# Performance work log

Measured on AMD Instinct MI355X. Metric: run time of the kernel, lower is better.

The kernel has to match this reference:

```python
import jax, jax.numpy as jnp
import numpy as np

N, D_IN, R, D_OUT, U = 500000, 128, 256, 64, 10000
EPS = 1e-8


def _vb_layer(m, v, W_mu, W_lv, relu_out):
    # Variational Bayes linear layer, moment propagation:
    #   out_mean = m @ W_mu
    #   out_var  = v @ (W_mu^2 + W_var) + m^2 @ W_var,  W_var = exp(W_lv)
    W_var = jnp.exp(W_lv)
    M = m @ W_mu
    V = v @ (W_mu * W_mu + W_var) + (m * m) @ W_var
    if relu_out:
        gate = (M > 0).astype(M.dtype)
        M = M * gate
        V = V * gate
    return M, V


def setup_inputs() -> dict:
    key = jax.random.key(0)
    ks = jax.random.split(key, 6)
    X = jax.random.normal(ks[0], (N, D_IN), jnp.float32)
    X_idx = jnp.sort(jax.random.randint(ks[1], (N,), 0, U, dtype=jnp.int32))
    W_mu0 = jax.random.normal(ks[2], (D_IN, R), jnp.float32) / np.sqrt(D_IN)
    W_lv0 = jax.random.normal(ks[3], (D_IN, R), jnp.float32) * 0.1 - 4.0
    W_mu1 = jax.random.normal(ks[4], (R, D_OUT), jnp.float32) / np.sqrt(R)
    W_lv1 = jax.random.normal(ks[5], (R, D_OUT), jnp.float32) * 0.1 - 4.0
    return {"X": X, "X_idx": X_idx, "W_mu0": W_mu0, "W_lv0": W_lv0,
            "W_mu1": W_mu1, "W_lv1": W_lv1}


def reference(X, X_idx, W_mu0, W_lv0, W_mu1, W_lv1):
    m, v = _vb_layer(X, jnp.zeros_like(X), W_mu0, W_lv0, True)   # [N, R]
    m, v = _vb_layer(m, v, W_mu1, W_lv1, False)                  # [N, D_OUT]
    v = jnp.maximum(v, EPS)
    inv_v = 1.0 / v
    # precision-weighted aggregation per group id (replaces per-uid loop)
    var_inv_sum = jax.ops.segment_sum(inv_v, X_idx, num_segments=U) + EPS
    mean_sum = jax.ops.segment_sum(m * inv_v, X_idx, num_segments=U)
    emb_var = 1.0 / var_inv_sum          # [U, D_OUT]
    emb_mean = mean_sum * emb_var        # [U, D_OUT]
    return emb_mean, emb_var
```

## Files before the change

### kernel.cpp

```cpp
#include <hip/hip_runtime.h>
#include <stdint.h>

#define N_ROWS 500000
#define U_DIM 10000
#define EPSV 1e-8f
#define NTILES 15625

typedef __attribute__((ext_vector_type(8))) short bf16x8;
typedef __attribute__((ext_vector_type(4))) float f32x4;

__device__ __forceinline__ short f2bf(float f) {
  unsigned u = __float_as_uint(f);
  u += 0x7fffu + ((u >> 16) & 1u);
  return (short)(u >> 16);
}
__device__ __forceinline__ float bf2f(short s) {
  return __uint_as_float(((unsigned)(unsigned short)s) << 16);
}

__global__ void prep_weights(const float* __restrict__ Wmu0,
                             const float* __restrict__ Wlv0,
                             const float* __restrict__ Wmu1,
                             const float* __restrict__ Wlv1,
                             short* __restrict__ wgt) {
  int i = blockIdx.x * blockDim.x + threadIdx.x;
  if (i < 32768) {
    int c = i & 255, k = i >> 8;
    int rc = c >> 5, ct = (c >> 4) & 1, n = c & 15;
    int kt = k >> 5, q = (k >> 3) & 3, u = k & 7;
    int lane = q * 16 + n;
    float mu = Wmu0[k * 256 + c];
    float ev = __expf(Wlv0[k * 256 + c]);
    wgt[((((rc * 2 + 0) * 2 + ct) * 4 + kt) * 64 + lane) * 8 + u] = f2bf(mu);
    wgt[((((rc * 2 + 1) * 2 + ct) * 4 + kt) * 64 + lane) * 8 + u] = f2bf(ev);
  } else if (i < 49152) {
    int i2 = i - 32768;
    int o = i2 & 63, j = i2 >> 6;
    int rc = j >> 5, q = (j >> 3) & 3, u = j & 7;
    int ct1 = o >> 4, n = o & 15;
    int lane = q * 16 + n;
    float mu = Wmu1[j * 64 + o];
    float ev = __expf(Wlv1[j * 64 + o]);
    int b = 65536 + (((rc * 4 + ct1) * 3 + 0) * 64 + lane) * 8 + u;
    wgt[b]        = f2bf(mu);
    wgt[b + 512]  = f2bf(mu * mu + ev);
    wgt[b + 1024] = f2bf(ev);
  }
}

__global__ __launch_bounds__(256, 2) void vb_fused(
    const float* __restrict__ X, const int* __restrict__ Xidx,
    const short* __restrict__ wgt, float* __restrict__ out) {
  __shared__ __align__(16) short stage[2][8192];
  __shared__ short ldsM[4][2][16 * 40];
  __shared__ short ldsV[4][2][16 * 40];

  const int tid  = threadIdx.x;
  const int w    = tid >> 6;
  const int lane = tid & 63;
  const int n    = lane & 15;
  const int q    = lane >> 4;
  const int T    = blockIdx.x * 4 + w;
  const bool active = (T < NTILES);
  const int row0 = active ? T * 32 : (N_ROWS - 32);

  const f32x4 zf4 = {0.f, 0.f, 0.f, 0.f};

  bf16x8 a_m[2][4], a_sq[2][4];
#pragma unroll
  for (int t = 0; t < 2; ++t) {
    const float* xr = X + (size_t)(row0 + t * 16 + n) * 128;
#pragma unroll
    for (int kt = 0; kt < 4; ++kt) {
      float xf[8];
      *(float4*)&xf[0] = *(const float4*)&xr[kt * 32 + q * 8];
      *(float4*)&xf[4] = *(const float4*)&xr[kt * 32 + q * 8 + 4];
#pragma unroll
      for (int u = 0; u < 8; ++u) {
        a_m[t][kt][u]  = f2bf(xf[u]);
        a_sq[t][kt][u] = f2bf(xf[u] * xf[u]);
      }
    }
  }

  f32x4 accm1[2][4], accv1[2][4];
#pragma unroll
  for (int t = 0; t < 2; ++t)
#pragma unroll
    for (int c = 0; c < 4; ++c) { accm1[t][c] = zf4; accv1[t][c] = zf4; }

  const uint4* g4 = (const uint4*)wgt;
  uint4 u0 = g4[tid], u1 = g4[tid + 256], u2 = g4[tid + 512], u3 = g4[tid + 768];

  const int lane8 = lane * 8;

#pragma unroll
  for (int rc = 0; rc < 8; ++rc) {
    uint4* s4 = (uint4*)&stage[rc & 1][0];
    s4[tid] = u0; s4[tid + 256] = u1; s4[tid + 512] = u2; s4[tid + 768] = u3;
    __syncthreads();
    if (rc < 7) {
      const uint4* gn = g4 + (rc + 1) * 1024;
      u0 = gn[tid]; u1 = gn[tid + 256]; u2 = gn[tid + 512]; u3 = gn[tid + 768];
    }

    const short* st = &stage[rc & 1][0];

    f32x4 accm0[2][2], accv0[2][2];
#pragma unroll
    for (int t = 0; t < 2; ++t)
#pragma unroll
      for (int c = 0; c < 2; ++c) { accm0[t][c] = zf4; accv0[t][c] = zf4; }

#pragma unroll
    for (int kt = 0; kt < 4; ++kt) {
#pragma unroll
      for (int ct = 0; ct < 2; ++ct) {
        bf16x8 bm = *(const bf16x8*)&st[((0 * 2 + ct) * 4 + kt) * 512 + lane8];
        bf16x8 bv = *(const bf16x8*)&st[((1 * 2 + ct) * 4 + kt) * 512 + lane8];
#pragma unroll
        for (int t = 0; t < 2; ++t) {
          accm0[t][ct] = __builtin_amdgcn_mfma_f32_16x16x32_bf16(a_m[t][kt],  bm, accm0[t][ct], 0, 0, 0);
          accv0[t][ct] = __builtin_amdgcn_mfma_f32_16x16x32_bf16(a_sq[t][kt], bv, accv0[t][ct], 0, 0, 0);
        }
      }
    }

#pragma unroll
    for (int t = 0; t < 2; ++t) {
#pragma unroll
      for (int ct = 0; ct < 2; ++ct) {
        const int c = ct * 16 + n;
#pragma unroll
        for (int reg = 0; reg < 4; ++reg) {
          float m = accm0[t][ct][reg], v = accv0[t][ct][reg];
          if (!(m > 0.f)) { m = 0.f; v = 0.f; }
          const int row = q * 4 + reg;
          ldsM[w][t][row * 40 + c] = f2bf(m);
          ldsV[w][t][row * 40 + c] = f2bf(v);
        }
      }
    }
    bf16x8 am[2], av[2], asq[2];
#pragma unroll
    for (int t = 0; t < 2; ++t) {
      am[t] = *(const bf16x8*)&ldsM[w][t][n * 40 + q * 8];
      av[t] = *(const bf16x8*)&ldsV[w][t][n * 40 + q * 8];
#pragma unroll
      for (int u = 0; u < 8; ++u) {
        float f = bf2f(am[t][u]);
        asq[t][u] = f2bf(f * f);
      }
    }

    const short* l1b = wgt + 65536 + rc * 6144 + lane8;
#pragma unroll
    for (int ct1 = 0; ct1 < 4; ++ct1) {
      const short* fb = l1b + ct1 * 1536;
      bf16x8 b1 = *(const bf16x8*)&fb[0];
      bf16x8 b2 = *(const bf16x8*)&fb[512];
      bf16x8 b3 = *(const bf16x8*)&fb[1024];
#pragma unroll
      for (int t = 0; t < 2; ++t) {
        accm1[t][ct1] = __builtin_amdgcn_mfma_f32_16x16x32_bf16(am[t],  b1, accm1[t][ct1], 0, 0, 0);
        accv1[t][ct1] = __builtin_amdgcn_mfma_f32_16x16x32_bf16(av[t],  b2, accv1[t][ct1], 0, 0, 0);
        accv1[t][ct1] = __builtin_amdgcn_mfma_f32_16x16x32_bf16(asq[t], b3, accv1[t][ct1], 0, 0, 0);
      }
    }
  }

  if (!active) return;
  float* meanp = out;
  float* varp  = out + U_DIM * 64;
#pragma unroll
  for (int t = 0; t < 2; ++t) {
    int4 idx4 = *(const int4*)&Xidx[row0 + t * 16 + q * 4];
    int uid[4] = {idx4.x, idx4.y, idx4.z, idx4.w};
#pragma unroll
    for (int ct = 0; ct < 4; ++ct) {
      const int o = ct * 16 + n;
      float sm = 0.f, sv = 0.f;
      int cur = uid[0];
#pragma unroll
      for (int reg = 0; reg < 4; ++reg) {
        float v1 = fmaxf(accv1[t][ct][reg], EPSV);
        float inv = 1.0f / v1;
        float mi  = accm1[t][ct][reg] * inv;
        if (uid[reg] != cur) {
          atomicAdd(&meanp[cur * 64 + o], sm);
          atomicAdd(&varp[cur * 64 + o], sv);
          sm = 0.f; sv = 0.f; cur = uid[reg];
        }
        sm += mi; sv += inv;
      }
      atomicAdd(&meanp[cur * 64 + o], sm);
      atomicAdd(&varp[cur * 64 + o], sv);
    }
  }
}

__global__ void finalize(float* __restrict__ out) {
  int i = blockIdx.x * blockDim.x + threadIdx.x;
  if (i < U_DIM * 64) {
    float s = out[U_DIM * 64 + i];
    float var = 1.0f / (s + EPSV);
    out[U_DIM * 64 + i] = var;
    out[i] = out[i] * var;
  }
}

extern "C" void kernel_launch(void* const* d_in, const int* in_sizes, int n_in,
                              void* d_out, int out_size, void* d_ws, size_t ws_size,
                              hipStream_t stream) {
  (void)in_sizes; (void)n_in; (void)out_size; (void)ws_size;
  const float* X    = (const float*)d_in[0];
  const int*   Xidx = (const int*)d_in[1];
  const float* Wmu0 = (const float*)d_in[2];
  const float* Wlv0 = (const float*)d_in[3];
  const float* Wmu1 = (const float*)d_in[4];
  const float* Wlv1 = (const float*)d_in[5];
  float* out = (float*)d_out;
  short* wgt = (short*)d_ws;

  hipMemsetAsync(d_out, 0, (size_t)U_DIM * 64 * 2 * sizeof(float), stream);
  prep_weights<<<192, 256, 0, stream>>>(Wmu0, Wlv0, Wmu1, Wlv1, wgt);
  vb_fused<<<3907, 256, 0, stream>>>(X, Xidx, wgt, out);
  finalize<<<(U_DIM * 64 + 255) / 256, 256, 0, stream>>>(out);
}
```

Measured before the change: 583.7 us.

## Halve per-wave row tile and stream layer-0 weights with global_load_lds

Each wave now processes 16 rows instead of 32, halving accumulator and A-fragment registers, and the grid doubles with launch bounds raised to 3 blocks per CU to increase occupancy. Layer-0 weight staging now uses direct global-to-LDS async loads instead of a register round trip. The trade-off is that every block re-streams the full weight set from L2 for half as many rows, doubling weight traffic and the per-row barrier overhead.

```diff
diff --git a/kernel.cpp b/kernel.cpp
--- a/kernel.cpp
+++ b/kernel.cpp
@@ -4,7 +4,7 @@
 #define N_ROWS 500000
 #define U_DIM 10000
 #define EPSV 1e-8f
-#define NTILES 15625
+#define NT16 31250
 
 typedef __attribute__((ext_vector_type(8))) short bf16x8;
 typedef __attribute__((ext_vector_type(4))) float f32x4;
@@ -48,12 +48,12 @@
   }
 }
 
-__global__ __launch_bounds__(256, 2) void vb_fused(
+__global__ __launch_bounds__(256, 3) void vb_fused(
     const float* __restrict__ X, const int* __restrict__ Xidx,
     const short* __restrict__ wgt, float* __restrict__ out) {
   __shared__ __align__(16) short stage[2][8192];
-  __shared__ short ldsM[4][2][16 * 40];
-  __shared__ short ldsV[4][2][16 * 40];
+  __shared__ __align__(16) short ldsM[4][16 * 40];
+  __shared__ __align__(16) short ldsV[4][16 * 40];
 
   const int tid  = threadIdx.x;
   const int w    = tid >> 6;
@@ -61,15 +61,15 @@
   const int n    = lane & 15;
   const int q    = lane >> 4;
   const int T    = blockIdx.x * 4 + w;
-  const bool active = (T < NTILES);
-  const int row0 = active ? T * 32 : (N_ROWS - 32);
+  const bool active = (T < NT16);
+  const int row0 = active ? T * 16 : (N_ROWS - 16);
 
   const f32x4 zf4 = {0.f, 0.f, 0.f, 0.f};
-
-  bf16x8 a_m[2][4], a_sq[2][4];
-#pragma unroll
-  for (int t = 0; t < 2; ++t) {
-    const float* xr = X + (size_t)(row0 + t * 16 + n) * 128;
+  const int lane8 = lane * 8;
+
+  bf16x8 a_m[4], a_sq[4];
+  {
+    const float* xr = X + (size_t)(row0 + n) * 128;
 #pragma unroll
     for (int kt = 0; kt < 4; ++kt) {
       float xf[8];
@@ -77,80 +77,71 @@
       *(float4*)&xf[4] = *(const float4*)&xr[kt * 32 + q * 8 + 4];
 #pragma unroll
       for (int u = 0; u < 8; ++u) {
-        a_m[t][kt][u]  = f2bf(xf[u]);
-        a_sq[t][kt][u] = f2bf(xf[u] * xf[u]);
-      }
-    }
-  }
-
-  f32x4 accm1[2][4], accv1[2][4];
-#pragma unroll
-  for (int t = 0; t < 2; ++t)
-#pragma unroll
-    for (int c = 0; c < 4; ++c) { accm1[t][c] = zf4; accv1[t][c] = zf4; }
-
-  const uint4* g4 = (const uint4*)wgt;
-  uint4 u0 = g4[tid], u1 = g4[tid + 256], u2 = g4[tid + 512], u3 = g4[tid + 768];
-
-  const int lane8 = lane * 8;
+        a_m[kt][u]  = f2bf(xf[u]);
+        a_sq[kt][u] = f2bf(xf[u] * xf[u]);
+      }
+    }
+  }
+
+  f32x4 accm1[4], accv1[4];
+#pragma unroll
+  for (int c = 0; c < 4; ++c) { accm1[c] = zf4; accv1[c] = zf4; }
+
+  const char* gbase = (const char*)wgt;
+#define ISSUE_STAGE(rc_, buf_)                                                 \
+  do {                                                                         \
+    _Pragma("unroll")                                                          \
+    for (int s_ = 0; s_ < 4; ++s_) {                                           \
+      __builtin_amdgcn_global_load_lds(                                        \
+          (const __attribute__((address_space(1))) unsigned int*)              \
+              (gbase + (rc_) * 16384 + s_ * 4096 + tid * 16),                  \
+          (__attribute__((address_space(3))) unsigned int*)                    \
+              ((char*)&stage[buf_][0] + s_ * 4096 + (w << 10)),                \
+          16, 0, 0);                                                           \
+    }                                                                          \
+  } while (0)
+
+  ISSUE_STAGE(0, 0);
 
 #pragma unroll
   for (int rc = 0; rc < 8; ++rc) {
-    uint4* s4 = (uint4*)&stage[rc & 1][0];
-    s4[tid] = u0; s4[tid + 256] = u1; s4[tid + 512] = u2; s4[tid + 768] = u3;
     __syncthreads();
-    if (rc < 7) {
-      const uint4* gn = g4 + (rc + 1) * 1024;
-      u0 = gn[tid]; u1 = gn[tid + 256]; u2 = gn[tid + 512]; u3 = gn[tid + 768];
-    }
+    if (rc < 7) ISSUE_STAGE(rc + 1, (rc + 1) & 1);
 
     const short* st = &stage[rc & 1][0];
 
-    f32x4 accm0[2][2], accv0[2][2];
-#pragma unroll
-    for (int t = 0; t < 2; ++t)
-#pragma unroll
-      for (int c = 0; c < 2; ++c) { accm0[t][c] = zf4; accv0[t][c] = zf4; }
-
+    f32x4 accm0[2], accv0[2];
+    accm0[0] = zf4; accm0[1] = zf4; accv0[0] = zf4; accv0[1] = zf4;
 #pragma unroll
     for (int kt = 0; kt < 4; ++kt) {
 #pragma unroll
       for (int ct = 0; ct < 2; ++ct) {
         bf16x8 bm = *(const bf16x8*)&st[((0 * 2 + ct) * 4 + kt) * 512 + lane8];
         bf16x8 bv = *(const bf16x8*)&st[((1 * 2 + ct) * 4 + kt) * 512 + lane8];
-#pragma unroll
-        for (int t = 0; t < 2; ++t) {
-          accm0[t][ct] = __builtin_amdgcn_mfma_f32_16x16x32_bf16(a_m[t][kt],  bm, accm0[t][ct], 0, 0, 0);
-          accv0[t][ct] = __builtin_amdgcn_mfma_f32_16x16x32_bf16(a_sq[t][kt], bv, accv0[t][ct], 0, 0, 0);
-        }
-      }
-    }
-
-#pragma unroll
-    for (int t = 0; t < 2; ++t) {
-#pragma unroll
-      for (int ct = 0; ct < 2; ++ct) {
-        const int c = ct * 16 + n;
-#pragma unroll
-        for (int reg = 0; reg < 4; ++reg) {
-          float m = accm0[t][ct][reg], v = accv0[t][ct][reg];
-          if (!(m > 0.f)) { m = 0.f; v = 0.f; }
-          const int row = q * 4 + reg;
-          ldsM[w][t][row * 40 + c] = f2bf(m);
-          ldsV[w][t][row * 40 + c] = f2bf(v);
-        }
-      }
-    }
-    bf16x8 am[2], av[2], asq[2];
-#pragma unroll
-    for (int t = 0; t < 2; ++t) {
-      am[t] = *(const bf16x8*)&ldsM[w][t][n * 40 + q * 8];
-      av[t] = *(const bf16x8*)&ldsV[w][t][n * 40 + q * 8];
-#pragma unroll
-      for (int u = 0; u < 8; ++u) {
-        float f = bf2f(am[t][u]);
-        asq[t][u] = f2bf(f * f);
-      }
+        accm0[ct] = __builtin_amdgcn_mfma_f32_16x16x32_bf16(a_m[kt],  bm, accm0[ct], 0, 0, 0);
+        accv0[ct] = __builtin_amdgcn_mfma_f32_16x16x32_bf16(a_sq[kt], bv, accv0[ct], 0, 0, 0);
+      }
+    }
+
+#pragma unroll
+    for (int ct = 0; ct < 2; ++ct) {
+      const int c = ct * 16 + n;
+#pragma unroll
+      for (int reg = 0; reg < 4; ++reg) {
+        float m = accm0[ct][reg], v = accv0[ct][reg];
+        if (!(m > 0.f)) { m = 0.f; v = 0.f; }
+        const int row = q * 4 + reg;
+        ldsM[w][row * 40 + c] = f2bf(m);
+        ldsV[w][row * 40 + c] = f2bf(v);
+      }
+    }
+    bf16x8 am = *(const bf16x8*)&ldsM[w][n * 40 + q * 8];
+    bf16x8 av = *(const bf16x8*)&ldsV[w][n * 40 + q * 8];
+    bf16x8 asq;
+#pragma unroll
+    for (int u = 0; u < 8; ++u) {
+      float f = bf2f(am[u]);
+      asq[u] = f2bf(f * f);
     }
 
     const short* l1b = wgt + 65536 + rc * 6144 + lane8;
@@ -160,42 +151,37 @@
       bf16x8 b1 = *(const bf16x8*)&fb[0];
       bf16x8 b2 = *(const bf16x8*)&fb[512];
       bf16x8 b3 = *(const bf16x8*)&fb[1024];
-#pragma unroll
-      for (int t = 0; t < 2; ++t) {
-        accm1[t][ct1] = __builtin_amdgcn_mfma_f32_16x16x32_bf16(am[t],  b1, accm1[t][ct1], 0, 0, 0);
-        accv1[t][ct1] = __builtin_amdgcn_mfma_f32_16x16x32_bf16(av[t],  b2, accv1[t][ct1], 0, 0, 0);
-        accv1[t][ct1] = __builtin_amdgcn_mfma_f32_16x16x32_bf16(asq[t], b3, accv1[t][ct1], 0, 0, 0);
-      }
-    }
-  }
+      accm1[ct1] = __builtin_amdgcn_mfma_f32_16x16x32_bf16(am,  b1, accm1[ct1], 0, 0, 0);
+      accv1[ct1] = __builtin_amdgcn_mfma_f32_16x16x32_bf16(av,  b2, accv1[ct1], 0, 0, 0);
+      accv1[ct1] = __builtin_amdgcn_mfma_f32_16x16x32_bf16(asq, b3, accv1[ct1], 0, 0, 0);
+    }
+  }
+#undef ISSUE_STAGE
 
   if (!active) return;
   float* meanp = out;
   float* varp  = out + U_DIM * 64;
-#pragma unroll
-  for (int t = 0; t < 2; ++t) {
-    int4 idx4 = *(const int4*)&Xidx[row0 + t * 16 + q * 4];
-    int uid[4] = {idx4.x, idx4.y, idx4.z, idx4.w};
-#pragma unroll
-    for (int ct = 0; ct < 4; ++ct) {
-      const int o = ct * 16 + n;
-      float sm = 0.f, sv = 0.f;
-      int cur = uid[0];
-#pragma unroll
-      for (int reg = 0; reg < 4; ++reg) {
-        float v1 = fmaxf(accv1[t][ct][reg], EPSV);
-        float inv = 1.0f / v1;
-        float mi  = accm1[t][ct][reg] * inv;
-        if (uid[reg] != cur) {
-          atomicAdd(&meanp[cur * 64 + o], sm);
-          atomicAdd(&varp[cur * 64 + o], sv);
-          sm = 0.f; sv = 0.f; cur = uid[reg];
-        }
-        sm += mi; sv += inv;
-      }
-      atomicAdd(&meanp[cur * 64 + o], sm);
-      atomicAdd(&varp[cur * 64 + o], sv);
-    }
+  int4 idx4 = *(const int4*)&Xidx[row0 + q * 4];
+  int uid[4] = {idx4.x, idx4.y, idx4.z, idx4.w};
+#pragma unroll
+  for (int ct = 0; ct < 4; ++ct) {
+    const int o = ct * 16 + n;
+    float sm = 0.f, sv = 0.f;
+    int cur = uid[0];
+#pragma unroll
+    for (int reg = 0; reg < 4; ++reg) {
+      float v1 = fmaxf(accv1[ct][reg], EPSV);
+      float inv = 1.0f / v1;
+      float mi  = accm1[ct][reg] * inv;
+      if (uid[reg] != cur) {
+        atomicAdd(&meanp[cur * 64 + o], sm);
+        atomicAdd(&varp[cur * 64 + o], sv);
+        sm = 0.f; sv = 0.f; cur = uid[reg];
+      }
+      sm += mi; sv += inv;
+    }
+    atomicAdd(&meanp[cur * 64 + o], sm);
+    atomicAdd(&varp[cur * 64 + o], sv);
   }
 }
 
@@ -224,6 +210,6 @@
 
   hipMemsetAsync(d_out, 0, (size_t)U_DIM * 64 * 2 * sizeof(float), stream);
   prep_weights<<<192, 256, 0, stream>>>(Wmu0, Wlv0, Wmu1, Wlv1, wgt);
-  vb_fused<<<3907, 256, 0, stream>>>(X, Xidx, wgt, out);
+  vb_fused<<<7813, 256, 0, stream>>>(X, Xidx, wgt, out);
   finalize<<<(U_DIM * 64 + 255) / 256, 256, 0, stream>>>(out);
 }
```

Measured after the change: 556.4 us. -4.7%, faster.
